# Performance work log

Hardware: AMD Instinct MI355X
Metric: run time of the kernel (lower is better)

Reference implementation:

```python
import jax, jax.numpy as jnp
import numpy as np

NUM_NODES = 50000
NUM_EDGES = 300000
WIDTH = 32
EDGE_DIM = 6
HIDDEN = 128


def setup_inputs() -> dict:
    key = jax.random.key(0)
    ks = jax.random.split(key, 6)
    x = jax.random.normal(ks[0], (NUM_NODES, WIDTH), dtype=jnp.float32)
    senders = jax.random.randint(ks[1], (NUM_EDGES,), 0, NUM_NODES, dtype=jnp.int32)
    receivers = jax.random.randint(ks[2], (NUM_EDGES,), 0, NUM_NODES, dtype=jnp.int32)
    edge_attr = jax.random.normal(ks[3], (NUM_EDGES, EDGE_DIM), dtype=jnp.float32)
    W1 = jax.random.normal(ks[4], (EDGE_DIM, HIDDEN), dtype=jnp.float32) * (1.0 / np.sqrt(EDGE_DIM))
    b1 = jnp.zeros((HIDDEN,), dtype=jnp.float32)
    W2 = jax.random.normal(ks[5], (HIDDEN, WIDTH * WIDTH), dtype=jnp.float32) * (1.0 / np.sqrt(HIDDEN))
    b2 = jnp.zeros((WIDTH * WIDTH,), dtype=jnp.float32)
    return {"x": x, "senders": senders, "receivers": receivers, "edge_attr": edge_attr,
            "W1": W1, "b1": b1, "W2": W2, "b2": b2}


def reference(x, senders, receivers, edge_attr, W1, b1, W2, b2):
    # Edge MLP producing per-edge (WIDTH, WIDTH) kernel matrices
    h = jax.nn.relu(edge_attr @ W1 + b1)                 # (E, HIDDEN)
    weight = (h @ W2 + b2).reshape(-1, WIDTH, WIDTH)     # (E, W, W)
    # Gather sender features and apply per-edge matmul: (1,W) @ (W,W) -> (W,)
    x_j = x[senders]                                     # (E, W)
    msgs = jnp.einsum('ew,ewv->ev', x_j, weight)         # (E, W)
    # Scatter-sum into receivers (aggr == 'sum')
    updated_x = jax.ops.segment_sum(msgs, receivers, num_segments=NUM_NODES)
    return updated_x
```

## Files before the change

kernel.cpp:

```cpp
#include <hip/hip_runtime.h>
#include <hip/hip_bf16.h>

#define E_EDGES 300000
#define N_NODES 50000
#define BE 256
#define NT 256
#define KC 256
#define NCHUNK 16
#define CHUNK_BYTES 16384
#define BIAS_OFF 262144
#define W1PK_OFF 264192
#define B1PK_OFF 267264

typedef _Float16 h2 __attribute__((ext_vector_type(2)));
typedef _Float16 h8 __attribute__((ext_vector_type(8)));
typedef float f32x16 __attribute__((ext_vector_type(16)));

static __device__ __forceinline__ unsigned short f2h(float f) {
  _Float16 h = (_Float16)f;
  return __builtin_bit_cast(unsigned short, h);
}
static __device__ __forceinline__ h2 cvt2(float a, float b) {
  auto r = __builtin_amdgcn_cvt_pkrtz(a, b);
  return __builtin_bit_cast(h2, r);
}
static __device__ __forceinline__ h2 bc(unsigned u) { return __builtin_bit_cast(h2, u); }
static __device__ __forceinline__ h2 dup_lo(h2 p) { return (h2){p[0], p[0]}; }
static __device__ __forceinline__ h2 dup_hi(h2 p) { return (h2){p[1], p[1]}; }
static __device__ __forceinline__ h8 mk4(h2 hd, const h2* p) {
  h2 m0 = hd * p[0], m1 = hd * p[1], m2 = hd * p[2], m3 = hd * p[3];
  return (h8){m0[0], m0[1], m1[0], m1[1], m2[0], m2[1], m3[0], m3[1]};
}
static __device__ __forceinline__ h8 pk4(const h2* p) {
  return (h8){p[0][0], p[0][1], p[1][0], p[1][1], p[2][0], p[2][1], p[3][0], p[3][1]};
}

__global__ void prep_w2t(const float* __restrict__ W2, const float* __restrict__ b2,
                         const float* __restrict__ W1, const float* __restrict__ b1,
                         char* __restrict__ ws) {
  int tid = blockIdx.x * 256 + threadIdx.x;
  if (tid < 65536) {
    int c   = tid >> 12;
    int rem = tid & 4095;
    int v   = rem >> 7;
    int kp  = rem & 127;
    int kg2 = c * KC + kp * 2;
    unsigned u = (unsigned)f2h(W2[(size_t)kg2 * 32 + v]) |
                 ((unsigned)f2h(W2[(size_t)(kg2 + 1) * 32 + v]) << 16);
    int off = c * CHUNK_BYTES + v * 512 + ((kp * 4) ^ ((v & 31) << 4));
    *(unsigned*)(ws + off) = u;
  } else if (tid < 66048) {
    int i  = tid - 65536;
    int v  = i & 31;
    int wp = i >> 5;
    int w  = wp * 2;
    unsigned u = (unsigned)f2h(b2[w * 32 + v]) |
                 ((unsigned)f2h(b2[(w + 1) * 32 + v]) << 16);
    *(unsigned*)(ws + BIAS_OFF + v * 64 + wp * 4) = u;
  } else if (tid < 66816) {
    int i = tid - 66048;
    unsigned short s = f2h(W1[i]);
    *(unsigned*)(ws + W1PK_OFF + i * 4) = (unsigned)s | ((unsigned)s << 16);
  } else if (tid < 66944) {
    int i = tid - 66816;
    unsigned short s = f2h(b1[i]);
    *(unsigned*)(ws + B1PK_OFF + i * 4) = (unsigned)s | ((unsigned)s << 16);
  }
}

__launch_bounds__(NT, 4)
__global__ void nnconv_main(const float* __restrict__ x,
                            const int* __restrict__ senders,
                            const int* __restrict__ receivers,
                            const float* __restrict__ edge_attr,
                            const char* __restrict__ ws,
                            float* __restrict__ out) {
  __shared__ __align__(16) char w2t[2][CHUNK_BYTES];
  __shared__ int rcv_lds[BE];

  const int t    = threadIdx.x;
  const int wid  = t >> 6;
  const int lane = t & 63;
  const int col  = lane & 31;
  const int hi   = lane >> 5;
  const int E0   = blockIdx.x * BE;

  {
#pragma unroll
    for (int it = 0; it < 4; ++it)
      __builtin_amdgcn_global_load_lds(
          (const __attribute__((address_space(1))) void*)(ws + it * 4096 + t * 16),
          (__attribute__((address_space(3))) void*)(&w2t[0][0] + it * 4096 + t * 16), 16, 0, 0);
  }

  rcv_lds[t] = (E0 + t < E_EDGES) ? receivers[E0 + t] : -1;

  const int el0 = wid * 64 + col;
  const int el1 = el0 + 32;
  const int ge0 = min(E0 + el0, E_EDGES - 1);
  const int ge1 = min(E0 + el1, E_EDGES - 1);

  h2 ea2[6];
  {
    const float2* p0 = (const float2*)(edge_attr + (size_t)ge0 * 6);
    const float2* p1 = (const float2*)(edge_attr + (size_t)ge1 * 6);
    const float2 a0 = p0[0], a1 = p0[1], a2 = p0[2];
    const float2 c0 = p1[0], c1 = p1[1], c2 = p1[2];
    ea2[0] = cvt2(a0.x, c0.x); ea2[1] = cvt2(a0.y, c0.y);
    ea2[2] = cvt2(a1.x, c1.x); ea2[3] = cvt2(a1.y, c1.y);
    ea2[4] = cvt2(a2.x, c2.x); ea2[5] = cvt2(a2.y, c2.y);
  }

  const float* row0 = x + (size_t)senders[ge0] * 32;
  const float* row1 = x + (size_t)senders[ge1] * 32;
  float4 fa, fb;
  fa = *(const float4*)(row0 + hi * 8);      fb = *(const float4*)(row0 + hi * 8 + 4);
  const h2 xA0[4] = {cvt2(fa.x, fa.y), cvt2(fa.z, fa.w), cvt2(fb.x, fb.y), cvt2(fb.z, fb.w)};
  fa = *(const float4*)(row0 + 16 + hi * 8); fb = *(const float4*)(row0 + 16 + hi * 8 + 4);
  const h2 xB0[4] = {cvt2(fa.x, fa.y), cvt2(fa.z, fa.w), cvt2(fb.x, fb.y), cvt2(fb.z, fb.w)};
  fa = *(const float4*)(row1 + hi * 8);      fb = *(const float4*)(row1 + hi * 8 + 4);
  const h2 xA1[4] = {cvt2(fa.x, fa.y), cvt2(fa.z, fa.w), cvt2(fb.x, fb.y), cvt2(fb.z, fb.w)};
  fa = *(const float4*)(row1 + 16 + hi * 8); fb = *(const float4*)(row1 + 16 + hi * 8 + 4);
  const h2 xB1[4] = {cvt2(fa.x, fa.y), cvt2(fa.z, fa.w), cvt2(fb.x, fb.y), cvt2(fb.z, fb.w)};

  const unsigned* w1p = (const unsigned*)(ws + W1PK_OFF);
  const unsigned* b1p = (const unsigned*)(ws + B1PK_OFF);

  __syncthreads();

  f32x16 acc0 = {};
  f32x16 acc1 = {};
  const int swB = (col & 31) << 4;
  int buf = 0;

#pragma unroll 1
  for (int c = 0; c < NCHUNK; ++c) {
    if (c + 1 < NCHUNK) {
      const char* g = ws + (c + 1) * CHUNK_BYTES;
      char* l = &w2t[buf ^ 1][0];
#pragma unroll
      for (int it = 0; it < 4; ++it)
        __builtin_amdgcn_global_load_lds(
            (const __attribute__((address_space(1))) void*)(g + it * 4096 + t * 16),
            (__attribute__((address_space(3))) void*)(l + it * 4096 + t * 16), 16, 0, 0);
    }

    h2 hv2[8];
    {
      const uint4* bq = (const uint4*)(b1p + c * 8);
      const uint4 b0 = bq[0], b4 = bq[1];
      hv2[0] = bc(b0.x); hv2[1] = bc(b0.y); hv2[2] = bc(b0.z); hv2[3] = bc(b0.w);
      hv2[4] = bc(b4.x); hv2[5] = bc(b4.y); hv2[6] = bc(b4.z); hv2[7] = bc(b4.w);
#pragma unroll
      for (int d = 0; d < 6; ++d) {
        const uint4* wq = (const uint4*)(w1p + d * 128 + c * 8);
        const uint4 w0 = wq[0], w4 = wq[1];
        hv2[0] += ea2[d] * bc(w0.x); hv2[1] += ea2[d] * bc(w0.y);
        hv2[2] += ea2[d] * bc(w0.z); hv2[3] += ea2[d] * bc(w0.w);
        hv2[4] += ea2[d] * bc(w4.x); hv2[5] += ea2[d] * bc(w4.y);
        hv2[6] += ea2[d] * bc(w4.z); hv2[7] += ea2[d] * bc(w4.w);
      }
    }
    h2 hdA[8], hdB[8];
#pragma unroll
    for (int kq = 0; kq < 8; ++kq) {
      h2 r = __builtin_elementwise_max(hv2[kq], (h2)(_Float16)0);
      hdA[kq] = dup_lo(r);
      hdB[kq] = dup_hi(r);
    }

    const char* Bb = &w2t[buf][0] + col * 512;
    __builtin_amdgcn_s_setprio(1);
#pragma unroll
    for (int s = 0; s < 16; ++s) {
      const h8 B = *(const h8*)(Bb + ((s * 32 + hi * 16) ^ swB));
      const int kq = s >> 1;
      h8 A0, A1;
      if (s & 1) { A0 = mk4(hdA[kq], xB0); A1 = mk4(hdB[kq], xB1); }
      else       { A0 = mk4(hdA[kq], xA0); A1 = mk4(hdB[kq], xA1); }
      acc0 = __builtin_amdgcn_mfma_f32_32x32x16_f16(A0, B, acc0, 0, 0, 0);
      acc1 = __builtin_amdgcn_mfma_f32_32x32x16_f16(A1, B, acc1, 0, 0, 0);
    }
    __builtin_amdgcn_s_setprio(0);
    __syncthreads();
    buf ^= 1;
  }

  {
    const char* bb = ws + BIAS_OFF + col * 64;
    const h8 B0 = *(const h8*)(bb + hi * 16);
    const h8 B1 = *(const h8*)(bb + 32 + hi * 16);
    acc0 = __builtin_amdgcn_mfma_f32_32x32x16_f16(pk4(xA0), B0, acc0, 0, 0, 0);
    acc1 = __builtin_amdgcn_mfma_f32_32x32x16_f16(pk4(xA1), B0, acc1, 0, 0, 0);
    acc0 = __builtin_amdgcn_mfma_f32_32x32x16_f16(pk4(xB0), B1, acc0, 0, 0, 0);
    acc1 = __builtin_amdgcn_mfma_f32_32x32x16_f16(pk4(xB1), B1, acc1, 0, 0, 0);
  }

#pragma unroll
  for (int r = 0; r < 16; ++r) {
    const int row = (r & 3) + 8 * (r >> 2) + 4 * hi;
    const int rcv0 = rcv_lds[wid * 64 + row];
    if (rcv0 >= 0) atomicAdd(out + (size_t)rcv0 * 32 + col, acc0[r]);
    const int rcv1 = rcv_lds[wid * 64 + 32 + row];
    if (rcv1 >= 0) atomicAdd(out + (size_t)rcv1 * 32 + col, acc1[r]);
  }
}

extern "C" void kernel_launch(void* const* d_in, const int* in_sizes, int n_in,
                              void* d_out, int out_size, void* d_ws, size_t ws_size,
                              hipStream_t stream) {
  const float* x         = (const float*)d_in[0];
  const int*   senders   = (const int*)d_in[1];
  const int*   receivers = (const int*)d_in[2];
  const float* edge_attr = (const float*)d_in[3];
  const float* W1        = (const float*)d_in[4];
  const float* b1        = (const float*)d_in[5];
  const float* W2        = (const float*)d_in[6];
  const float* b2        = (const float*)d_in[7];
  float* out = (float*)d_out;
  char*  ws  = (char*)d_ws;

  (void)hipMemsetAsync(out, 0, (size_t)N_NODES * 32 * sizeof(float), stream);
  prep_w2t<<<262, 256, 0, stream>>>(W2, b2, W1, b1, ws);
  nnconv_main<<<(E_EDGES + BE - 1) / BE, NT, 0, stream>>>(
      x, senders, receivers, edge_attr, ws, out);
}
```

Measured before the change: 117.2 us.

## Split hidden dimension across grid and process 128 edges per wave

Each block now covers 512 edges, and each wave computes four 32-edge MFMA tiles that share every W2 chunk read from LDS, so each LDS B-load feeds more MFMAs. The hidden reduction is split across a second grid dimension: each block handles 8 of the 16 chunks and adds its partial result with atomics, and only the first half adds the bias. Hidden activations are computed once per edge and exchanged across lanes with shuffles. The cost is more registers (launch bounds lowered to 3), twice as many output atomics, and extra shuffle work.

```diff
diff --git a/kernel.cpp b/kernel.cpp
--- a/kernel.cpp
+++ b/kernel.cpp
@@ -3,11 +3,11 @@
 
 #define E_EDGES 300000
 #define N_NODES 50000
-#define BE 256
+#define BE 512
 #define NT 256
 #define KC 256
-#define NCHUNK 16
 #define CHUNK_BYTES 16384
+#define CPB 8
 #define BIAS_OFF 262144
 #define W1PK_OFF 264192
 #define B1PK_OFF 267264
@@ -24,9 +24,13 @@
   auto r = __builtin_amdgcn_cvt_pkrtz(a, b);
   return __builtin_bit_cast(h2, r);
 }
-static __device__ __forceinline__ h2 bc(unsigned u) { return __builtin_bit_cast(h2, u); }
-static __device__ __forceinline__ h2 dup_lo(h2 p) { return (h2){p[0], p[0]}; }
-static __device__ __forceinline__ h2 dup_hi(h2 p) { return (h2){p[1], p[1]}; }
+static __device__ __forceinline__ h2 bcu(unsigned u) { return __builtin_bit_cast(h2, u); }
+static __device__ __forceinline__ h2 dup_lo(unsigned u) {
+  h2 p = bcu(u); return (h2){p[0], p[0]};
+}
+static __device__ __forceinline__ h2 dup_hi(unsigned u) {
+  h2 p = bcu(u); return (h2){p[1], p[1]};
+}
 static __device__ __forceinline__ h8 mk4(h2 hd, const h2* p) {
   h2 m0 = hd * p[0], m1 = hd * p[1], m2 = hd * p[2], m3 = hd * p[3];
   return (h8){m0[0], m0[1], m1[0], m1[1], m2[0], m2[1], m3[0], m3[1]};
@@ -68,7 +72,7 @@
   }
 }
 
-__launch_bounds__(NT, 4)
+__launch_bounds__(NT, 3)
 __global__ void nnconv_main(const float* __restrict__ x,
                             const int* __restrict__ senders,
                             const int* __restrict__ receivers,
@@ -84,58 +88,62 @@
   const int col  = lane & 31;
   const int hi   = lane >> 5;
   const int E0   = blockIdx.x * BE;
-
-  {
-#pragma unroll
-    for (int it = 0; it < 4; ++it)
-      __builtin_amdgcn_global_load_lds(
-          (const __attribute__((address_space(1))) void*)(ws + it * 4096 + t * 16),
-          (__attribute__((address_space(3))) void*)(&w2t[0][0] + it * 4096 + t * 16), 16, 0, 0);
-  }
-
-  rcv_lds[t] = (E0 + t < E_EDGES) ? receivers[E0 + t] : -1;
-
-  const int el0 = wid * 64 + col;
-  const int el1 = el0 + 32;
-  const int ge0 = min(E0 + el0, E_EDGES - 1);
-  const int ge1 = min(E0 + el1, E_EDGES - 1);
-
+  const int kh   = blockIdx.y;
+  const int c0   = kh * CPB;
+
+#pragma unroll
+  for (int it = 0; it < 4; ++it)
+    __builtin_amdgcn_global_load_lds(
+        (const __attribute__((address_space(1))) void*)(ws + c0 * CHUNK_BYTES + it * 4096 + t * 16),
+        (__attribute__((address_space(3))) void*)(&w2t[0][0] + it * 4096 + t * 16), 16, 0, 0);
+
+#pragma unroll
+  for (int i = t; i < BE; i += NT)
+    rcv_lds[i] = (E0 + i < E_EDGES) ? receivers[E0 + i] : -1;
+
+  const int wb = wid * 128;
+
+  const int geL = min(E0 + wb + lane, E_EDGES - 1);
+  const int geH = min(E0 + wb + 64 + lane, E_EDGES - 1);
   h2 ea2[6];
   {
-    const float2* p0 = (const float2*)(edge_attr + (size_t)ge0 * 6);
-    const float2* p1 = (const float2*)(edge_attr + (size_t)ge1 * 6);
+    const float2* p0 = (const float2*)(edge_attr + (size_t)geL * 6);
+    const float2* p1 = (const float2*)(edge_attr + (size_t)geH * 6);
     const float2 a0 = p0[0], a1 = p0[1], a2 = p0[2];
-    const float2 c0 = p1[0], c1 = p1[1], c2 = p1[2];
-    ea2[0] = cvt2(a0.x, c0.x); ea2[1] = cvt2(a0.y, c0.y);
-    ea2[2] = cvt2(a1.x, c1.x); ea2[3] = cvt2(a1.y, c1.y);
-    ea2[4] = cvt2(a2.x, c2.x); ea2[5] = cvt2(a2.y, c2.y);
-  }
-
-  const float* row0 = x + (size_t)senders[ge0] * 32;
-  const float* row1 = x + (size_t)senders[ge1] * 32;
-  float4 fa, fb;
-  fa = *(const float4*)(row0 + hi * 8);      fb = *(const float4*)(row0 + hi * 8 + 4);
-  const h2 xA0[4] = {cvt2(fa.x, fa.y), cvt2(fa.z, fa.w), cvt2(fb.x, fb.y), cvt2(fb.z, fb.w)};
-  fa = *(const float4*)(row0 + 16 + hi * 8); fb = *(const float4*)(row0 + 16 + hi * 8 + 4);
-  const h2 xB0[4] = {cvt2(fa.x, fa.y), cvt2(fa.z, fa.w), cvt2(fb.x, fb.y), cvt2(fb.z, fb.w)};
-  fa = *(const float4*)(row1 + hi * 8);      fb = *(const float4*)(row1 + hi * 8 + 4);
-  const h2 xA1[4] = {cvt2(fa.x, fa.y), cvt2(fa.z, fa.w), cvt2(fb.x, fb.y), cvt2(fb.z, fb.w)};
-  fa = *(const float4*)(row1 + 16 + hi * 8); fb = *(const float4*)(row1 + 16 + hi * 8 + 4);
-  const h2 xB1[4] = {cvt2(fa.x, fa.y), cvt2(fa.z, fa.w), cvt2(fb.x, fb.y), cvt2(fb.z, fb.w)};
+    const float2 c0f = p1[0], c1f = p1[1], c2f = p1[2];
+    ea2[0] = cvt2(a0.x, c0f.x); ea2[1] = cvt2(a0.y, c0f.y);
+    ea2[2] = cvt2(a1.x, c1f.x); ea2[3] = cvt2(a1.y, c1f.y);
+    ea2[4] = cvt2(a2.x, c2f.x); ea2[5] = cvt2(a2.y, c2f.y);
+  }
+
+  h2 xA[4][4], xB[4][4];
+#pragma unroll
+  for (int g = 0; g < 4; ++g) {
+    const int ge = min(E0 + wb + g * 32 + col, E_EDGES - 1);
+    const float* row = x + (size_t)senders[ge] * 32;
+    float4 fa = *(const float4*)(row + hi * 8);
+    float4 fb = *(const float4*)(row + hi * 8 + 4);
+    xA[g][0] = cvt2(fa.x, fa.y); xA[g][1] = cvt2(fa.z, fa.w);
+    xA[g][2] = cvt2(fb.x, fb.y); xA[g][3] = cvt2(fb.z, fb.w);
+    fa = *(const float4*)(row + 16 + hi * 8);
+    fb = *(const float4*)(row + 16 + hi * 8 + 4);
+    xB[g][0] = cvt2(fa.x, fa.y); xB[g][1] = cvt2(fa.z, fa.w);
+    xB[g][2] = cvt2(fb.x, fb.y); xB[g][3] = cvt2(fb.z, fb.w);
+  }
 
   const unsigned* w1p = (const unsigned*)(ws + W1PK_OFF);
   const unsigned* b1p = (const unsigned*)(ws + B1PK_OFF);
 
   __syncthreads();
 
-  f32x16 acc0 = {};
-  f32x16 acc1 = {};
+  f32x16 acc0 = {}, acc1 = {}, acc2 = {}, acc3 = {};
   const int swB = (col & 31) << 4;
   int buf = 0;
 
 #pragma unroll 1
-  for (int c = 0; c < NCHUNK; ++c) {
-    if (c + 1 < NCHUNK) {
+  for (int ci = 0; ci < CPB; ++ci) {
+    const int c = c0 + ci;
+    if (ci + 1 < CPB) {
       const char* g = ws + (c + 1) * CHUNK_BYTES;
       char* l = &w2t[buf ^ 1][0];
 #pragma unroll
@@ -145,64 +153,83 @@
             (__attribute__((address_space(3))) void*)(l + it * 4096 + t * 16), 16, 0, 0);
     }
 
-    h2 hv2[8];
+    unsigned hp[8];
     {
+      h2 hv[8];
       const uint4* bq = (const uint4*)(b1p + c * 8);
       const uint4 b0 = bq[0], b4 = bq[1];
-      hv2[0] = bc(b0.x); hv2[1] = bc(b0.y); hv2[2] = bc(b0.z); hv2[3] = bc(b0.w);
-      hv2[4] = bc(b4.x); hv2[5] = bc(b4.y); hv2[6] = bc(b4.z); hv2[7] = bc(b4.w);
+      hv[0] = bcu(b0.x); hv[1] = bcu(b0.y); hv[2] = bcu(b0.z); hv[3] = bcu(b0.w);
+      hv[4] = bcu(b4.x); hv[5] = bcu(b4.y); hv[6] = bcu(b4.z); hv[7] = bcu(b4.w);
 #pragma unroll
       for (int d = 0; d < 6; ++d) {
         const uint4* wq = (const uint4*)(w1p + d * 128 + c * 8);
         const uint4 w0 = wq[0], w4 = wq[1];
-        hv2[0] += ea2[d] * bc(w0.x); hv2[1] += ea2[d] * bc(w0.y);
-        hv2[2] += ea2[d] * bc(w0.z); hv2[3] += ea2[d] * bc(w0.w);
-        hv2[4] += ea2[d] * bc(w4.x); hv2[5] += ea2[d] * bc(w4.y);
-        hv2[6] += ea2[d] * bc(w4.z); hv2[7] += ea2[d] * bc(w4.w);
+        hv[0] += ea2[d] * bcu(w0.x); hv[1] += ea2[d] * bcu(w0.y);
+        hv[2] += ea2[d] * bcu(w0.z); hv[3] += ea2[d] * bcu(w0.w);
+        hv[4] += ea2[d] * bcu(w4.x); hv[5] += ea2[d] * bcu(w4.y);
+        hv[6] += ea2[d] * bcu(w4.z); hv[7] += ea2[d] * bcu(w4.w);
+      }
+#pragma unroll
+      for (int kq = 0; kq < 8; ++kq)
+        hp[kq] = __builtin_bit_cast(unsigned,
+                   __builtin_elementwise_max(hv[kq], (h2)(_Float16)0));
+    }
+
+    const char* Bb = &w2t[buf][0] + col * 512;
+    h2 hd0, hd1, hd2, hd3;
+#pragma unroll
+    for (int s = 0; s < 16; ++s) {
+      const int kq = s >> 1;
+      if ((s & 1) == 0) {
+        const unsigned u0 = __shfl(hp[kq], col);
+        const unsigned u1 = __shfl(hp[kq], col + 32);
+        hd0 = dup_lo(u0);
+        hd1 = dup_lo(u1);
+        hd2 = dup_hi(u0);
+        hd3 = dup_hi(u1);
+      }
+      const h8 B = *(const h8*)(Bb + ((s * 32 + hi * 16) ^ swB));
+      if (s & 1) {
+        acc0 = __builtin_amdgcn_mfma_f32_32x32x16_f16(mk4(hd0, xB[0]), B, acc0, 0, 0, 0);
+        acc1 = __builtin_amdgcn_mfma_f32_32x32x16_f16(mk4(hd1, xB[1]), B, acc1, 0, 0, 0);
+        acc2 = __builtin_amdgcn_mfma_f32_32x32x16_f16(mk4(hd2, xB[2]), B, acc2, 0, 0, 0);
+        acc3 = __builtin_amdgcn_mfma_f32_32x32x16_f16(mk4(hd3, xB[3]), B, acc3, 0, 0, 0);
+      } else {
+        acc0 = __builtin_amdgcn_mfma_f32_32x32x16_f16(mk4(hd0, xA[0]), B, acc0, 0, 0, 0);
+        acc1 = __builtin_amdgcn_mfma_f32_32x32x16_f16(mk4(hd1, xA[1]), B, acc1, 0, 0, 0);
+        acc2 = __builtin_amdgcn_mfma_f32_32x32x16_f16(mk4(hd2, xA[2]), B, acc2, 0, 0, 0);
+        acc3 = __builtin_amdgcn_mfma_f32_32x32x16_f16(mk4(hd3, xA[3]), B, acc3, 0, 0, 0);
       }
     }
-    h2 hdA[8], hdB[8];
-#pragma unroll
-    for (int kq = 0; kq < 8; ++kq) {
-      h2 r = __builtin_elementwise_max(hv2[kq], (h2)(_Float16)0);
-      hdA[kq] = dup_lo(r);
-      hdB[kq] = dup_hi(r);
-    }
-
-    const char* Bb = &w2t[buf][0] + col * 512;
-    __builtin_amdgcn_s_setprio(1);
-#pragma unroll
-    for (int s = 0; s < 16; ++s) {
-      const h8 B = *(const h8*)(Bb + ((s * 32 + hi * 16) ^ swB));
-      const int kq = s >> 1;
-      h8 A0, A1;
-      if (s & 1) { A0 = mk4(hdA[kq], xB0); A1 = mk4(hdB[kq], xB1); }
-      else       { A0 = mk4(hdA[kq], xA0); A1 = mk4(hdB[kq], xA1); }
-      acc0 = __builtin_amdgcn_mfma_f32_32x32x16_f16(A0, B, acc0, 0, 0, 0);
-      acc1 = __builtin_amdgcn_mfma_f32_32x32x16_f16(A1, B, acc1, 0, 0, 0);
-    }
-    __builtin_amdgcn_s_setprio(0);
     __syncthreads();
     buf ^= 1;
   }
 
-  {
+  if (kh == 0) {
     const char* bb = ws + BIAS_OFF + col * 64;
     const h8 B0 = *(const h8*)(bb + hi * 16);
     const h8 B1 = *(const h8*)(bb + 32 + hi * 16);
-    acc0 = __builtin_amdgcn_mfma_f32_32x32x16_f16(pk4(xA0), B0, acc0, 0, 0, 0);
-    acc1 = __builtin_amdgcn_mfma_f32_32x32x16_f16(pk4(xA1), B0, acc1, 0, 0, 0);
-    acc0 = __builtin_amdgcn_mfma_f32_32x32x16_f16(pk4(xB0), B1, acc0, 0, 0, 0);
-    acc1 = __builtin_amdgcn_mfma_f32_32x32x16_f16(pk4(xB1), B1, acc1, 0, 0, 0);
+    acc0 = __builtin_amdgcn_mfma_f32_32x32x16_f16(pk4(xA[0]), B0, acc0, 0, 0, 0);
+    acc1 = __builtin_amdgcn_mfma_f32_32x32x16_f16(pk4(xA[1]), B0, acc1, 0, 0, 0);
+    acc2 = __builtin_amdgcn_mfma_f32_32x32x16_f16(pk4(xA[2]), B0, acc2, 0, 0, 0);
+    acc3 = __builtin_amdgcn_mfma_f32_32x32x16_f16(pk4(xA[3]), B0, acc3, 0, 0, 0);
+    acc0 = __builtin_amdgcn_mfma_f32_32x32x16_f16(pk4(xB[0]), B1, acc0, 0, 0, 0);
+    acc1 = __builtin_amdgcn_mfma_f32_32x32x16_f16(pk4(xB[1]), B1, acc1, 0, 0, 0);
+    acc2 = __builtin_amdgcn_mfma_f32_32x32x16_f16(pk4(xB[2]), B1, acc2, 0, 0, 0);
+    acc3 = __builtin_amdgcn_mfma_f32_32x32x16_f16(pk4(xB[3]), B1, acc3, 0, 0, 0);
   }
 
 #pragma unroll
   for (int r = 0; r < 16; ++r) {
     const int row = (r & 3) + 8 * (r >> 2) + 4 * hi;
-    const int rcv0 = rcv_lds[wid * 64 + row];
-    if (rcv0 >= 0) atomicAdd(out + (size_t)rcv0 * 32 + col, acc0[r]);
-    const int rcv1 = rcv_lds[wid * 64 + 32 + row];
-    if (rcv1 >= 0) atomicAdd(out + (size_t)rcv1 * 32 + col, acc1[r]);
+    const int r0 = rcv_lds[wb + row];
+    if (r0 >= 0) atomicAdd(out + (size_t)r0 * 32 + col, acc0[r]);
+    const int r1 = rcv_lds[wb + 32 + row];
+    if (r1 >= 0) atomicAdd(out + (size_t)r1 * 32 + col, acc1[r]);
+    const int r2 = rcv_lds[wb + 64 + row];
+    if (r2 >= 0) atomicAdd(out + (size_t)r2 * 32 + col, acc2[r]);
+    const int r3 = rcv_lds[wb + 96 + row];
+    if (r3 >= 0) atomicAdd(out + (size_t)r3 * 32 + col, acc3[r]);
   }
 }
 
@@ -222,6 +249,7 @@
 
   (void)hipMemsetAsync(out, 0, (size_t)N_NODES * 32 * sizeof(float), stream);
   prep_w2t<<<262, 256, 0, stream>>>(W2, b2, W1, b1, ws);
-  nnconv_main<<<(E_EDGES + BE - 1) / BE, NT, 0, stream>>>(
+  dim3 grid((E_EDGES + BE - 1) / BE, 2);
+  nnconv_main<<<grid, NT, 0, stream>>>(
       x, senders, receivers, edge_attr, ws, out);
 }
```

Result: slower. 121.7 us (+3.9%).
